# Kernel optimization log

Hardware: AMD Instinct MI355X
Metric: run time of the kernel (lower is better)

Reference implementation:

```python
import jax, jax.numpy as jnp
import numpy as np

KERNEL_SIZE = 7
CHANNELS = 3

def _box_filter(x):
    # Depthwise uniform box filter, 'same' padding (pad = k//2, k odd).
    k = KERNEL_SIZE
    kernel = jnp.full((CHANNELS, 1, k, k), 1.0 / (k * k), dtype=x.dtype)
    return jax.lax.conv_general_dilated(
        x, kernel,
        window_strides=(1, 1),
        padding=[(k // 2, k // 2), (k // 2, k // 2)],
        dimension_numbers=('NCHW', 'OIHW', 'NCHW'),
        feature_group_count=CHANNELS)

def setup_inputs() -> dict:
    key = jax.random.key(0)
    k1, k2 = jax.random.split(key)
    shape = (32, 3, 512, 512)
    pred = jax.random.normal(k1, shape, dtype=jnp.float32)
    target = jax.random.normal(k2, shape, dtype=jnp.float32)
    return {"pred": pred, "target": target}

def reference(pred, target):
    pred_contrast = pred - _box_filter(pred)
    target_contrast = target - _box_filter(target)
    return jnp.mean(jnp.abs(pred_contrast - target_contrast))
```

## Files before the change

### kernel.cpp

```cpp
#include <hip/hip_runtime.h>

namespace {
constexpr int H = 512;
constexpr int W = 512;
constexpr int NC = 96;
constexpr int RSTRIP = 32;
constexpr int SPP = H / RSTRIP;
constexpr int NBLK = NC * SPP;
constexpr int NTHR = 512;
constexpr int TROWS = RSTRIP + 6;
constexpr int LROW = W + 8;
constexpr int NF4 = TROWS * (W / 4);
constexpr float INV_K2 = 1.0f / 49.0f;
constexpr float INV_TOTAL = 1.0f / (32.0f * 3.0f * 512.0f * 512.0f);
}

template <int P8, int P4, bool EMIT>
__device__ __forceinline__ void step(const float* __restrict__ lds_row,
                                     float (&hr)[8], float (&dr)[4],
                                     float& vs, float& acc)
{
    const float w0 = lds_row[0];
    const float w1 = lds_row[1];
    const float w2 = lds_row[2];
    const float w3 = lds_row[3];
    const float w4 = lds_row[4];
    const float w5 = lds_row[5];
    const float w6 = lds_row[6];
    const float h = ((w0 + w1) + (w2 + w3)) + ((w4 + w5) + w6);

    constexpr int S  = P8 & 7;
    constexpr int So = (P8 + 1) & 7;
    constexpr int Q  = P4 & 3;
    constexpr int Qo = (P4 + 1) & 3;

    vs += h - hr[So];
    hr[S] = h;
    if (EMIT) acc += fabsf(dr[Qo] - vs * INV_K2);
    dr[Q] = w3;
}

__global__ __launch_bounds__(NTHR, 4) void lcl_partial(
    const float4* __restrict__ pred4, const float4* __restrict__ targ4,
    float* __restrict__ partials)
{
    __shared__ float sm[TROWS * LROW + 8];

    const int t     = threadIdx.x;
    const int plane = blockIdx.x >> 4;
    const int y0    = (blockIdx.x & 15) * RSTRIP;
    const int base4 = plane * (H * (W / 4));

    if (t < TROWS * 6) {
        const int r = t / 6;
        const int k = t - 6 * r;
        sm[r * LROW + (k < 3 ? 1 + k : 513 + k)] = 0.f;
    }

#pragma unroll
    for (int it = 0; it < 10; ++it) {
        const int i = t + it * NTHR;
        if (it < 9 || i < NF4) {
            const int r  = i >> 7;
            const int cw = i & 127;
            const int y  = y0 - 3 + r;
            float4 d4 = make_float4(0.f, 0.f, 0.f, 0.f);
            if ((unsigned)y < (unsigned)H) {
                const float4 a = pred4[base4 + y * (W / 4) + cw];
                const float4 b = targ4[base4 + y * (W / 4) + cw];
                d4 = make_float4(a.x - b.x, a.y - b.y, a.z - b.z, a.w - b.w);
            }
            *(float4*)&sm[r * LROW + 4 + 4 * cw] = d4;
        }
    }
    __syncthreads();

    float hr[8], dr[4];
#pragma unroll
    for (int s = 0; s < 8; ++s) hr[s] = 0.f;
#pragma unroll
    for (int s = 0; s < 4; ++s) dr[s] = 0.f;
    float vs = 0.f, acc = 0.f;

    const float* p = &sm[t + 1];

    step<0, 0, false>(p + 0 * LROW, hr, dr, vs, acc);
    step<1, 1, false>(p + 1 * LROW, hr, dr, vs, acc);
    step<2, 2, false>(p + 2 * LROW, hr, dr, vs, acc);
    step<3, 3, false>(p + 3 * LROW, hr, dr, vs, acc);
    step<4, 0, false>(p + 4 * LROW, hr, dr, vs, acc);
    step<5, 1, false>(p + 5 * LROW, hr, dr, vs, acc);

#pragma unroll 1
    for (int b = 0; b < 4; ++b) {
        const float* q = p + (6 + 8 * b) * LROW;
        step<6, 2, true>(q + 0 * LROW, hr, dr, vs, acc);
        step<7, 3, true>(q + 1 * LROW, hr, dr, vs, acc);
        step<0, 0, true>(q + 2 * LROW, hr, dr, vs, acc);
        step<1, 1, true>(q + 3 * LROW, hr, dr, vs, acc);
        step<2, 2, true>(q + 4 * LROW, hr, dr, vs, acc);
        step<3, 3, true>(q + 5 * LROW, hr, dr, vs, acc);
        step<4, 0, true>(q + 6 * LROW, hr, dr, vs, acc);
        step<5, 1, true>(q + 7 * LROW, hr, dr, vs, acc);
    }

#pragma unroll
    for (int off = 32; off > 0; off >>= 1)
        acc += __shfl_down(acc, off, 64);
    float* wred = &sm[TROWS * LROW];
    if ((t & 63) == 0) wred[t >> 6] = acc;
    __syncthreads();
    if (t == 0) {
        float s = ((wred[0] + wred[1]) + (wred[2] + wred[3]))
                + ((wred[4] + wred[5]) + (wred[6] + wred[7]));
        partials[blockIdx.x] = s;
    }
}

__global__ __launch_bounds__(256) void lcl_reduce(const float* __restrict__ partials,
                                                  float* __restrict__ out)
{
    __shared__ float wred[4];
    const int tid = threadIdx.x;
    float s = 0.0f;
    for (int i = tid; i < NBLK; i += 256) s += partials[i];
#pragma unroll
    for (int off = 32; off > 0; off >>= 1)
        s += __shfl_down(s, off, 64);
    if ((tid & 63) == 0) wred[tid >> 6] = s;
    __syncthreads();
    if (tid == 0) out[0] = ((wred[0] + wred[1]) + (wred[2] + wred[3])) * INV_TOTAL;
}

extern "C" void kernel_launch(void* const* d_in, const int* in_sizes, int n_in,
                              void* d_out, int out_size, void* d_ws, size_t ws_size,
                              hipStream_t stream) {
    const float4* pred4 = (const float4*)d_in[0];
    const float4* targ4 = (const float4*)d_in[1];
    float* out      = (float*)d_out;
    float* partials = (float*)d_ws;

    lcl_partial<<<NBLK, NTHR, 0, stream>>>(pred4, targ4, partials);
    lcl_reduce<<<1, 256, 0, stream>>>(partials, out);
}
```

Baseline: 47.69 us.

## Compute four adjacent columns per thread with float4 LDS reads and sliding horizontal sums

Each thread now handles four adjacent output columns over an 8-row segment instead of one column over all 32 rows. Three float4 LDS loads replace seven scalar loads per row, and the horizontal sums for neighbouring columns are updated incrementally rather than recomputed. This cuts LDS traffic and add count per output. In exchange, each thread must warm up six extra rows per 8-row segment, which repeats vertical work, and register use rises from the 8x4 and 4x4 ring buffers.

Result: slower. 55.64 us (+16.7%).

```diff
diff --git a/kernel.cpp b/kernel.cpp
--- a/kernel.cpp
+++ b/kernel.cpp
@@ -16,28 +16,37 @@
 }
 
 template <int P8, int P4, bool EMIT>
-__device__ __forceinline__ void step(const float* __restrict__ lds_row,
-                                     float (&hr)[8], float (&dr)[4],
-                                     float& vs, float& acc)
+__device__ __forceinline__ void step4(const float* __restrict__ rowp,
+                                      float (&hr)[8][4], float (&dr)[4][4],
+                                      float (&vs)[4], float& acc)
 {
-    const float w0 = lds_row[0];
-    const float w1 = lds_row[1];
-    const float w2 = lds_row[2];
-    const float w3 = lds_row[3];
-    const float w4 = lds_row[4];
-    const float w5 = lds_row[5];
-    const float w6 = lds_row[6];
-    const float h = ((w0 + w1) + (w2 + w3)) + ((w4 + w5) + w6);
+    const float4 A = *(const float4*)(rowp);
+    const float4 B = *(const float4*)(rowp + 4);
+    const float4 C = *(const float4*)(rowp + 8);
+
+    const float h0 = ((A.y + A.z) + (A.w + B.x)) + ((B.y + B.z) + B.w);
+    const float h1 = h0 - A.y + C.x;
+    const float h2 = h1 - A.z + C.y;
+    const float h3 = h2 - A.w + C.z;
 
     constexpr int S  = P8 & 7;
     constexpr int So = (P8 + 1) & 7;
     constexpr int Q  = P4 & 3;
     constexpr int Qo = (P4 + 1) & 3;
 
-    vs += h - hr[So];
-    hr[S] = h;
-    if (EMIT) acc += fabsf(dr[Qo] - vs * INV_K2);
-    dr[Q] = w3;
+    vs[0] += h0 - hr[So][0]; hr[S][0] = h0;
+    vs[1] += h1 - hr[So][1]; hr[S][1] = h1;
+    vs[2] += h2 - hr[So][2]; hr[S][2] = h2;
+    vs[3] += h3 - hr[So][3]; hr[S][3] = h3;
+
+    if (EMIT) {
+        acc += fabsf(dr[Qo][0] - vs[0] * INV_K2)
+             + fabsf(dr[Qo][1] - vs[1] * INV_K2)
+             + fabsf(dr[Qo][2] - vs[2] * INV_K2)
+             + fabsf(dr[Qo][3] - vs[3] * INV_K2);
+    }
+
+    dr[Q][0] = B.x; dr[Q][1] = B.y; dr[Q][2] = B.z; dr[Q][3] = B.w;
 }
 
 __global__ __launch_bounds__(NTHR, 4) void lcl_partial(
@@ -75,33 +84,36 @@
     }
     __syncthreads();
 
-    float hr[8], dr[4];
+    const int g = t >> 7;
+    const int k = t & 127;
+
+    float hr[8][4], dr[4][4], vs[4];
 #pragma unroll
-    for (int s = 0; s < 8; ++s) hr[s] = 0.f;
+    for (int s = 0; s < 8; ++s) { hr[s][0]=0.f; hr[s][1]=0.f; hr[s][2]=0.f; hr[s][3]=0.f; }
 #pragma unroll
-    for (int s = 0; s < 4; ++s) dr[s] = 0.f;
-    float vs = 0.f, acc = 0.f;
+    for (int s = 0; s < 4; ++s) { dr[s][0]=0.f; dr[s][1]=0.f; dr[s][2]=0.f; dr[s][3]=0.f; }
+    vs[0]=0.f; vs[1]=0.f; vs[2]=0.f; vs[3]=0.f;
+    float acc = 0.f;
 
-    const float* p = &sm[t + 1];
+    const float* p = &sm[(8 * g) * LROW + 4 * k];
 
-    step<0, 0, false>(p + 0 * LROW, hr, dr, vs, acc);
-    step<1, 1, false>(p + 1 * LROW, hr, dr, vs, acc);
-    step<2, 2, false>(p + 2 * LROW, hr, dr, vs, acc);
-    step<3, 3, false>(p + 3 * LROW, hr, dr, vs, acc);
-    step<4, 0, false>(p + 4 * LROW, hr, dr, vs, acc);
-    step<5, 1, false>(p + 5 * LROW, hr, dr, vs, acc);
+    step4<0, 0, false>(p + 0 * LROW, hr, dr, vs, acc);
+    step4<1, 1, false>(p + 1 * LROW, hr, dr, vs, acc);
+    step4<2, 2, false>(p + 2 * LROW, hr, dr, vs, acc);
+    step4<3, 3, false>(p + 3 * LROW, hr, dr, vs, acc);
+    step4<4, 0, false>(p + 4 * LROW, hr, dr, vs, acc);
+    step4<5, 1, false>(p + 5 * LROW, hr, dr, vs, acc);
 
-#pragma unroll 1
-    for (int b = 0; b < 4; ++b) {
-        const float* q = p + (6 + 8 * b) * LROW;
-        step<6, 2, true>(q + 0 * LROW, hr, dr, vs, acc);
-        step<7, 3, true>(q + 1 * LROW, hr, dr, vs, acc);
-        step<0, 0, true>(q + 2 * LROW, hr, dr, vs, acc);
-        step<1, 1, true>(q + 3 * LROW, hr, dr, vs, acc);
-        step<2, 2, true>(q + 4 * LROW, hr, dr, vs, acc);
-        step<3, 3, true>(q + 5 * LROW, hr, dr, vs, acc);
-        step<4, 0, true>(q + 6 * LROW, hr, dr, vs, acc);
-        step<5, 1, true>(q + 7 * LROW, hr, dr, vs, acc);
+    {
+        const float* q = p + 6 * LROW;
+        step4<6, 2, true>(q + 0 * LROW, hr, dr, vs, acc);
+        step4<7, 3, true>(q + 1 * LROW, hr, dr, vs, acc);
+        step4<0, 0, true>(q + 2 * LROW, hr, dr, vs, acc);
+        step4<1, 1, true>(q + 3 * LROW, hr, dr, vs, acc);
+        step4<2, 2, true>(q + 4 * LROW, hr, dr, vs, acc);
+        step4<3, 3, true>(q + 5 * LROW, hr, dr, vs, acc);
+        step4<4, 0, true>(q + 6 * LROW, hr, dr, vs, acc);
+        step4<5, 1, true>(q + 7 * LROW, hr, dr, vs, acc);
     }
 
 #pragma unroll
```
